# Optimization experiments

Measured on AMD Instinct MI355X. Metric: run time of the kernel, lower is better.

## Reference

```python
import jax, jax.numpy as jnp
import numpy as np
from jax.scipy.special import betaln

B, T = 4096, 8192

def setup_inputs() -> dict:
    key = jax.random.key(0)
    k_obs, k_a1, k_b1, k_a2, k_b2 = jax.random.split(key, 5)
    obs_seq = (jax.random.uniform(k_obs, (B, T)) < 0.5).astype(jnp.float32)
    # priors strictly positive, away from 0 to keep betaln finite
    alpha1 = jax.random.uniform(k_a1, (B,)) * 2.0 + 0.5
    beta1 = jax.random.uniform(k_b1, (B,)) * 2.0 + 0.5
    alpha2 = jax.random.uniform(k_a2, (B,)) * 2.0 + 0.5
    beta2 = jax.random.uniform(k_b2, (B,)) * 2.0 + 0.5
    mixweight = jnp.float32(0.4)
    return {"obs_seq": obs_seq, "alpha1": alpha1, "beta1": beta1,
            "alpha2": alpha2, "beta2": beta2, "mixweight": mixweight}

def reference(obs_seq, alpha1, beta1, alpha2, beta2, mixweight):
    # cumulative successes/failures, shifted right by one (posterior BEFORE obs t)
    cs = jnp.cumsum(obs_seq, axis=1)          # [B,T]
    cf = jnp.cumsum(1.0 - obs_seq, axis=1)    # [B,T]
    s_prev = jnp.pad(cs[:, :-1], ((0, 0), (1, 0)))  # cat([0, cs[:-1]])
    f_prev = jnp.pad(cf[:, :-1], ((0, 0), (1, 0)))
    a1 = alpha1[:, None] + s_prev
    b1 = beta1[:, None] + f_prev
    a2 = alpha2[:, None] + s_prev
    b2 = beta2[:, None] + f_prev
    clog1 = betaln(a1, b1) - betaln(alpha1, beta1)[:, None]
    clog2 = betaln(a2, b2) - betaln(alpha2, beta2)[:, None]
    bigconst = -clog1
    c1 = mixweight * jnp.exp(clog1 + bigconst)
    c2 = (1.0 - mixweight) * jnp.exp(clog2 + bigconst)
    post_mixweight = c1 / (c1 + c2)
    # stack the post_dict entries into one [5,B,T] array
    return jnp.stack([a1, b1, a2, b2, post_mixweight])
```

## Files before the change

### kernel.cpp

```cpp
#include <hip/hip_runtime.h>


#define BLOCK 256
#define VEC 4

typedef float v4f __attribute__((ext_vector_type(4)));

__global__ __launch_bounds__(BLOCK) void bbm_kernel(
    const float* __restrict__ obs,
    const float* __restrict__ alpha1, const float* __restrict__ beta1,
    const float* __restrict__ alpha2, const float* __restrict__ beta2,
    const float* __restrict__ mixw,
    float* __restrict__ out,
    int T, size_t bt)
{
    const int row  = blockIdx.x;
    const int tid  = threadIdx.x;
    const int lane = tid & 63;
    const int wid  = tid >> 6;

    __shared__ int   sPart[4];
    __shared__ float dPart[4];

    const float A1 = alpha1[row], B1 = beta1[row];
    const float A2 = alpha2[row], B2 = beta2[row];
    const float w  = mixw[0];
    const float AB1 = A1 + B1, AB2 = A2 + B2;
    const float w2 = 1.0f - w;

    const float* __restrict__ orow = obs + (size_t)row * T;
    float* __restrict__ obase = out + (size_t)row * T;

    const unsigned long long lt_mask = ((unsigned long long)1 << lane) - 1;

    int   carry_s = 0;
    float carry_d = 0.0f;

    const int EPB  = BLOCK * VEC;
    const int segs = T / EPB;

    v4f cur = *(const v4f*)(orow + tid * VEC);

    for (int seg = 0; seg < segs; ++seg) {
        const int t0 = seg * EPB + tid * VEC;

        v4f nxt;
        if (seg + 1 < segs) nxt = *(const v4f*)(orow + (seg + 1) * EPB + tid * VEC);

        int bit[VEC], sloc[VEC];
        int ts = 0;
        #pragma unroll
        for (int j = 0; j < VEC; ++j) { bit[j] = cur[j] > 0.5f; sloc[j] = ts; ts += bit[j]; }

        unsigned long long m0 = __ballot(bit[0]);
        unsigned long long m1 = __ballot(bit[1]);
        unsigned long long m2 = __ballot(bit[2]);
        unsigned long long m3 = __ballot(bit[3]);
        const int wave_excl = __builtin_popcountll(m0 & lt_mask)
                            + __builtin_popcountll(m1 & lt_mask)
                            + __builtin_popcountll(m2 & lt_mask)
                            + __builtin_popcountll(m3 & lt_mask);
        const int wave_tot  = __builtin_popcountll(m0) + __builtin_popcountll(m1)
                            + __builtin_popcountll(m2) + __builtin_popcountll(m3);
        if (lane == 0) sPart[wid] = wave_tot;
        __syncthreads();
        int prior = 0, total = 0;
        #pragma unroll
        for (int wI = 0; wI < 4; ++wI) {
            int p = sPart[wI];
            total += p;
            if (wI < wid) prior += p;
        }
        const int tbase_s = carry_s + prior + wave_excl;

        float dloc[VEC];
        float td = 0.0f;
        #pragma unroll
        for (int j = 0; j < VEC; ++j) {
            const float ft = (float)(t0 + j);
            const float fs = (float)(tbase_s + sloc[j]);
            const float fp = ft - fs;
            const float sel1 = bit[j] ? (A1 + fs) : (B1 + fp);
            const float sel2 = bit[j] ? (A2 + fs) : (B2 + fp);
            const float delta = __logf(sel2 * (AB1 + ft)) - __logf(sel1 * (AB2 + ft));
            dloc[j] = td;
            td += delta;
        }

        float incl_d = td;
        #pragma unroll
        for (int off = 1; off < 64; off <<= 1) {
            float n = __shfl_up(incl_d, off, 64);
            if (lane >= off) incl_d += n;
        }
        if (lane == 63) dPart[wid] = incl_d;
        __syncthreads();
        float priord = 0.0f, totald = 0.0f;
        #pragma unroll
        for (int wI = 0; wI < 4; ++wI) {
            float p = dPart[wI];
            totald += p;
            if (wI < wid) priord += p;
        }
        const float tbase_d = carry_d + priord + (incl_d - td);

        v4f va1, vb1, va2, vb2, vpm;
        #pragma unroll
        for (int j = 0; j < VEC; ++j) {
            const float ft = (float)(t0 + j);
            const float fs = (float)(tbase_s + sloc[j]);
            const float fp = ft - fs;
            const float d  = tbase_d + dloc[j];
            va1[j] = A1 + fs;
            vb1[j] = B1 + fp;
            va2[j] = A2 + fs;
            vb2[j] = B2 + fp;
            vpm[j] = w / (w + w2 * __expf(d));
        }
        float* p = obase + t0;
        __builtin_nontemporal_store(va1, (v4f*)(p));
        __builtin_nontemporal_store(vb1, (v4f*)(p + bt));
        __builtin_nontemporal_store(va2, (v4f*)(p + 2 * bt));
        __builtin_nontemporal_store(vb2, (v4f*)(p + 3 * bt));
        __builtin_nontemporal_store(vpm, (v4f*)(p + 4 * bt));

        carry_s += total;
        carry_d += totald;
        cur = nxt;
    }
}

extern "C" void kernel_launch(void* const* d_in, const int* in_sizes, int n_in,
                              void* d_out, int out_size, void* d_ws, size_t ws_size,
                              hipStream_t stream) {
    const float* obs    = (const float*)d_in[0];
    const float* alpha1 = (const float*)d_in[1];
    const float* beta1  = (const float*)d_in[2];
    const float* alpha2 = (const float*)d_in[3];
    const float* beta2  = (const float*)d_in[4];
    const float* mixw   = (const float*)d_in[5];

    const int Bn = in_sizes[1];
    const int Tn = in_sizes[0] / Bn;
    const size_t bt = (size_t)Bn * (size_t)Tn;

    bbm_kernel<<<Bn, BLOCK, 0, stream>>>(obs, alpha1, beta1, alpha2, beta2,
                                         mixw, (float*)d_out, Tn, bt);
}
```

Baseline: 760.4 us.

## Assign one wavefront per row to remove block-level scan barriers

Each row is now scanned by a single 64-lane wavefront instead of a 256-thread block, with four rows per block. This drops the shared-memory partials and the two __syncthreads per segment, and the segment carry comes from a shuffle of lane 63. The four count outputs are now stored before the log-delta scan so their writes can overlap that work. In exchange each wave walks its row serially over four times as many segments, which lengthens the dependency chain per row, and each wave's loads and stores now cover 1KB per segment instead of 4KB.

```diff
diff --git a/kernel.cpp b/kernel.cpp
--- a/kernel.cpp
+++ b/kernel.cpp
@@ -14,13 +14,9 @@
     float* __restrict__ out,
     int T, size_t bt)
 {
-    const int row  = blockIdx.x;
-    const int tid  = threadIdx.x;
-    const int lane = tid & 63;
-    const int wid  = tid >> 6;
-
-    __shared__ int   sPart[4];
-    __shared__ float dPart[4];
+    const int lane = threadIdx.x & 63;
+    const int wid  = threadIdx.x >> 6;
+    const int row  = blockIdx.x * 4 + wid;
 
     const float A1 = alpha1[row], B1 = beta1[row];
     const float A2 = alpha2[row], B2 = beta2[row];
@@ -36,16 +32,16 @@
     int   carry_s = 0;
     float carry_d = 0.0f;
 
-    const int EPB  = BLOCK * VEC;
-    const int segs = T / EPB;
+    const int SEG  = 64 * VEC;
+    const int segs = T / SEG;
 
-    v4f cur = *(const v4f*)(orow + tid * VEC);
+    v4f cur = *(const v4f*)(orow + lane * VEC);
 
     for (int seg = 0; seg < segs; ++seg) {
-        const int t0 = seg * EPB + tid * VEC;
+        const int t0 = seg * SEG + lane * VEC;
 
         v4f nxt;
-        if (seg + 1 < segs) nxt = *(const v4f*)(orow + (seg + 1) * EPB + tid * VEC);
+        if (seg + 1 < segs) nxt = *(const v4f*)(orow + (seg + 1) * SEG + lane * VEC);
 
         int bit[VEC], sloc[VEC];
         int ts = 0;
@@ -62,26 +58,34 @@
                             + __builtin_popcountll(m3 & lt_mask);
         const int wave_tot  = __builtin_popcountll(m0) + __builtin_popcountll(m1)
                             + __builtin_popcountll(m2) + __builtin_popcountll(m3);
-        if (lane == 0) sPart[wid] = wave_tot;
-        __syncthreads();
-        int prior = 0, total = 0;
+        const int tbase_s = carry_s + wave_excl;
+
+        float fsv[VEC], fpv[VEC];
+        v4f va1, vb1, va2, vb2;
         #pragma unroll
-        for (int wI = 0; wI < 4; ++wI) {
-            int p = sPart[wI];
-            total += p;
-            if (wI < wid) prior += p;
+        for (int j = 0; j < VEC; ++j) {
+            const float ft = (float)(t0 + j);
+            const float fs = (float)(tbase_s + sloc[j]);
+            const float fp = ft - fs;
+            fsv[j] = fs; fpv[j] = fp;
+            va1[j] = A1 + fs;
+            vb1[j] = B1 + fp;
+            va2[j] = A2 + fs;
+            vb2[j] = B2 + fp;
         }
-        const int tbase_s = carry_s + prior + wave_excl;
+        float* p = obase + t0;
+        __builtin_nontemporal_store(va1, (v4f*)(p));
+        __builtin_nontemporal_store(vb1, (v4f*)(p + bt));
+        __builtin_nontemporal_store(va2, (v4f*)(p + 2 * bt));
+        __builtin_nontemporal_store(vb2, (v4f*)(p + 3 * bt));
 
         float dloc[VEC];
         float td = 0.0f;
         #pragma unroll
         for (int j = 0; j < VEC; ++j) {
             const float ft = (float)(t0 + j);
-            const float fs = (float)(tbase_s + sloc[j]);
-            const float fp = ft - fs;
-            const float sel1 = bit[j] ? (A1 + fs) : (B1 + fp);
-            const float sel2 = bit[j] ? (A2 + fs) : (B2 + fp);
+            const float sel1 = bit[j] ? (A1 + fsv[j]) : (B1 + fpv[j]);
+            const float sel2 = bit[j] ? (A2 + fsv[j]) : (B2 + fpv[j]);
             const float delta = __logf(sel2 * (AB1 + ft)) - __logf(sel1 * (AB2 + ft));
             dloc[j] = td;
             td += delta;
@@ -93,39 +97,19 @@
             float n = __shfl_up(incl_d, off, 64);
             if (lane >= off) incl_d += n;
         }
-        if (lane == 63) dPart[wid] = incl_d;
-        __syncthreads();
-        float priord = 0.0f, totald = 0.0f;
-        #pragma unroll
-        for (int wI = 0; wI < 4; ++wI) {
-            float p = dPart[wI];
-            totald += p;
-            if (wI < wid) priord += p;
-        }
-        const float tbase_d = carry_d + priord + (incl_d - td);
+        const float tbase_d  = carry_d + (incl_d - td);
+        const float total_d  = __shfl(incl_d, 63, 64);
 
-        v4f va1, vb1, va2, vb2, vpm;
+        v4f vpm;
         #pragma unroll
         for (int j = 0; j < VEC; ++j) {
-            const float ft = (float)(t0 + j);
-            const float fs = (float)(tbase_s + sloc[j]);
-            const float fp = ft - fs;
-            const float d  = tbase_d + dloc[j];
-            va1[j] = A1 + fs;
-            vb1[j] = B1 + fp;
-            va2[j] = A2 + fs;
-            vb2[j] = B2 + fp;
+            const float d = tbase_d + dloc[j];
             vpm[j] = w / (w + w2 * __expf(d));
         }
-        float* p = obase + t0;
-        __builtin_nontemporal_store(va1, (v4f*)(p));
-        __builtin_nontemporal_store(vb1, (v4f*)(p + bt));
-        __builtin_nontemporal_store(va2, (v4f*)(p + 2 * bt));
-        __builtin_nontemporal_store(vb2, (v4f*)(p + 3 * bt));
         __builtin_nontemporal_store(vpm, (v4f*)(p + 4 * bt));
 
-        carry_s += total;
-        carry_d += totald;
+        carry_s += wave_tot;
+        carry_d += total_d;
         cur = nxt;
     }
 }
@@ -144,6 +128,6 @@
     const int Tn = in_sizes[0] / Bn;
     const size_t bt = (size_t)Bn * (size_t)Tn;
 
-    bbm_kernel<<<Bn, BLOCK, 0, stream>>>(obs, alpha1, beta1, alpha2, beta2,
-                                         mixw, (float*)d_out, Tn, bt);
+    bbm_kernel<<<Bn / 4, BLOCK, 0, stream>>>(obs, alpha1, beta1, alpha2, beta2,
+                                             mixw, (float*)d_out, Tn, bt);
 }
```

Result: no change. 764.8 us (+0.6%).
